# Optimization experiments

Hardware: AMD Instinct MI355X
Metric: run time of the kernel (lower is better)

Reference implementation:

```python
import jax, jax.numpy as jnp
import numpy as np

B, T_IN, T_OUT, F, H = 256, 336, 96, 32, 256


def _lstm_cell(x_t, h, c, Wih, Whh, b):
    # PyTorch gate order: input, forget, cell(g), output
    gates = x_t @ Wih.T + h @ Whh.T + b  # [B, 4H]
    i, f, g, o = jnp.split(gates, 4, axis=-1)
    c_new = jax.nn.sigmoid(f) * c + jax.nn.sigmoid(i) * jnp.tanh(g)
    h_new = jax.nn.sigmoid(o) * jnp.tanh(c_new)
    return h_new, c_new


def setup_inputs() -> dict:
    key = jax.random.key(0)
    ks = jax.random.split(key, 16)
    s = 0.05  # keep recurrence numerically tame
    g = lambda k, shape: (jax.random.normal(k, shape) * s).astype(jnp.float32)
    return {
        "x": jax.random.normal(ks[0], (B, T_IN, F), dtype=jnp.float32),
        "enc_Wih0": g(ks[1], (4 * H, F)),
        "enc_Whh0": g(ks[2], (4 * H, H)),
        "enc_b0": g(ks[3], (4 * H,)),
        "enc_Wih1": g(ks[4], (4 * H, H)),
        "enc_Whh1": g(ks[5], (4 * H, H)),
        "enc_b1": g(ks[6], (4 * H,)),
        "dec_Wih0": g(ks[7], (4 * H, F)),
        "dec_Whh0": g(ks[8], (4 * H, H)),
        "dec_b0": g(ks[9], (4 * H,)),
        "dec_Wih1": g(ks[10], (4 * H, H)),
        "dec_Whh1": g(ks[11], (4 * H, H)),
        "dec_b1": g(ks[12], (4 * H,)),
        "dec_Wout": g(ks[13], (F, H)),
        "dec_bout": g(ks[14], (F,)),
    }


def reference(x, enc_Wih0, enc_Whh0, enc_b0, enc_Wih1, enc_Whh1, enc_b1,
              dec_Wih0, dec_Whh0, dec_b0, dec_Wih1, dec_Whh1, dec_b1,
              dec_Wout, dec_bout):
    batch = x.shape[0]
    zeros = jnp.zeros((batch, H), dtype=x.dtype)

    # --- encoder: step-by-step 2-layer LSTM over input sequence ---
    def enc_step(carry, x_t):
        h0, c0, h1, c1 = carry
        h0, c0 = _lstm_cell(x_t, h0, c0, enc_Wih0, enc_Whh0, enc_b0)
        h1, c1 = _lstm_cell(h0, h1, c1, enc_Wih1, enc_Whh1, enc_b1)
        return (h0, c0, h1, c1), None

    xs = jnp.swapaxes(x, 0, 1)  # [T_IN, B, F]
    (h0, c0, h1, c1), _ = jax.lax.scan(enc_step, (zeros, zeros, zeros, zeros), xs)

    def dec_step(carry, _):
        h0, c0, h1, c1, y = carry
        h0, c0 = _lstm_cell(y, h0, c0, dec_Wih0, dec_Whh0, dec_b0)
        h1, c1 = _lstm_cell(h0, h1, c1, dec_Wih1, dec_Whh1, dec_b1)
        y = h1 @ dec_Wout.T + dec_bout  # project hidden -> feature dim
        return (h0, c0, h1, c1, y), y

    y0 = x[:, -1, :]  # [B, F]
    _, ys = jax.lax.scan(dec_step, (h0, c0, h1, c1, y0), None, length=T_OUT)
    return jnp.swapaxes(ys, 0, 1)  # [B, T_OUT, F]
```

## Files before the change

### kernel.cpp

```cpp
#include <hip/hip_runtime.h>
#include <hip/hip_bf16.h>

#define BB   256
#define TIN  336
#define TOUT 96
#define FF   32
#define HH   256

#define NGS 16
#define NBG 16
#define RPG 16
#define TPB 512

#define KB0 9
#define KB1 16
#define ASTRIDE 520
#define XSTRIDE 40

#define N_L0  (16*4*KB0*64*8)
#define N_L1  (16*4*KB1*64*8)
#define U_E0  0
#define U_E1  (U_E0 + N_L0)
#define U_D0  (U_E1 + N_L1)
#define U_D1  (U_D0 + N_L1)
#define U_END (U_D1 + N_L1)
#define HPAR  65536
#define U_H0  U_END
#define U_H1  (U_H0 + 2*HPAR)
#define U_HD  (U_H1 + 2*HPAR)
#define U_CTR (U_HD + 96*HPAR)
#define U_ZEND (U_CTR + 2048)

#define GATE(bias, g, r, cc) (bias[(g)*16 + (cc)] + pbuf[0][r][(g)*16 + (cc)] + pbuf[1][r][(g)*16 + (cc)])

typedef __bf16 bf16x8 __attribute__((ext_vector_type(8)));
typedef float  f32x4  __attribute__((ext_vector_type(4)));

__device__ __forceinline__ float sigf(float x) { return 1.f / (1.f + __expf(-x)); }
__device__ __forceinline__ float tanhfast(float x) { return 1.f - 2.f / (__expf(2.f * x) + 1.f); }
__device__ __forceinline__ unsigned short f2bf(float f) {
    union { float f; unsigned u; } v; v.f = f;
    unsigned r = v.u + 0x7FFF + ((v.u >> 16) & 1);
    return (unsigned short)(r >> 16);
}
__device__ __forceinline__ uint4 ldg_sc(const void* p) {
    uint4 v;
    asm volatile("global_load_dwordx4 %0, %1, off sc0 sc1\n\ts_waitcnt vmcnt(0)"
                 : "=v"(v) : "v"(p) : "memory");
    return v;
}
__device__ __forceinline__ void ldg_sc2(const void* p0, const void* p1, uint4& a, uint4& b) {
    asm volatile("global_load_dwordx4 %0, %2, off sc0 sc1\n\t"
                 "global_load_dwordx4 %1, %3, off sc0 sc1\n\t"
                 "s_waitcnt vmcnt(0)"
                 : "=v"(a), "=v"(b) : "v"(p0), "v"(p1) : "memory");
}

__global__ void prep_kernel(const float* __restrict__ eWih0, const float* __restrict__ eWhh0,
                            const float* __restrict__ eWih1, const float* __restrict__ eWhh1,
                            const float* __restrict__ dWih0, const float* __restrict__ dWhh0,
                            const float* __restrict__ dWih1, const float* __restrict__ dWhh1,
                            const float* __restrict__ Wout,  float* __restrict__ wsf)
{
    unsigned short* wsu = (unsigned short*)wsf;
    for (long u = (long)blockIdx.x * blockDim.x + threadIdx.x; u < (long)U_END;
         u += (long)gridDim.x * blockDim.x) {
        int region; long l;
        if (u < U_E1)      { region = 0; l = u - U_E0; }
        else if (u < U_D0) { region = 1; l = u - U_E1; }
        else if (u < U_D1) { region = 2; l = u - U_D0; }
        else               { region = 3; l = u - U_D1; }
        const int KB = (region == 0) ? KB0 : KB1;
        int j = (int)(l & 7), lane = (int)((l >> 3) & 63);
        long rem = l >> 9;
        int kb = (int)(rem % KB), q = (int)(rem / KB);
        int nt = q & 3, gi = q >> 2;
        int k  = kb * 32 + ((lane >> 4) << 3) + j;
        int gj = nt * 256 + gi * 16 + (lane & 15);
        float v;
        if (region == 0)      v = (k < 32)  ? eWih0[gj * 32 + k]  : eWhh0[gj * 256 + (k - 32)];
        else if (region == 1) v = (k < 256) ? eWih1[gj * 256 + k] : eWhh1[gj * 256 + (k - 256)];
        else if (region == 2) {
            if (k < 256) v = dWhh0[gj * 256 + k];
            else {
                float acc = 0.f; int kk = k - 256;
                #pragma unroll 8
                for (int f = 0; f < 32; ++f) acc += dWih0[gj * 32 + f] * Wout[f * 256 + kk];
                v = acc;
            }
        } else                v = (k < 256) ? dWih1[gj * 256 + k] : dWhh1[gj * 256 + (k - 256)];
        wsu[u] = f2bf(v);
    }
    for (long z = (long)blockIdx.x * blockDim.x + threadIdx.x; z < (long)(4 * HPAR);
         z += (long)gridDim.x * blockDim.x)
        wsu[U_H0 + z] = 0;
    for (long z = (long)blockIdx.x * blockDim.x + threadIdx.x; z < 2048;
         z += (long)gridDim.x * blockDim.x)
        wsu[U_CTR + z] = 0;
}

__global__ __launch_bounds__(TPB) void lstm_main(
    const float* __restrict__ x,
    const float* __restrict__ eb0, const float* __restrict__ eb1,
    const float* __restrict__ db0, const float* __restrict__ db1,
    const float* __restrict__ Wout, const float* __restrict__ bout,
    const float* __restrict__ dWih0,
    float* __restrict__ ws, float* __restrict__ out)
{
    const int gi = blockIdx.x >> 4;
    const int gb = blockIdx.x & 15;

    unsigned short* wsu = (unsigned short*)ws;
    const unsigned short* h0u = wsu + U_H0;
    const unsigned short* h1u = wsu + U_H1;
    const unsigned short* hdu = wsu + U_HD;
    unsigned* h0d = (unsigned*)(wsu + U_H0);
    unsigned* hdd = (unsigned*)(wsu + U_HD);
    unsigned* flg = (unsigned*)(wsu + U_CTR) + gb * 32;

    const int t  = threadIdx.x;
    const int wv = t >> 6;
    const int ln = t & 63;
    const int nt = wv & 3, w2 = wv >> 2;
    const int arow = ln & 15, ak = (ln >> 4) << 3;

    __shared__ __align__(16) unsigned short Atile[16 * ASTRIDE];
    __shared__ __align__(16) unsigned short Xtile[16 * XSTRIDE];
    __shared__ float pbuf[2][16][68];
    __shared__ float cst[2][16][16];
    __shared__ float sb[5][64];

    if (t < 64) {
        int gj = (t >> 4) * 256 + gi * 16 + (t & 15);
        sb[0][t] = eb0[gj]; sb[1][t] = eb1[gj]; sb[3][t] = db1[gj]; sb[4][t] = db0[gj];
        float be = db0[gj];
        #pragma unroll 8
        for (int f = 0; f < 32; ++f) be += dWih0[gj * 32 + f] * bout[f];
        sb[2][t] = be;
    }
    if (t < 256) { cst[0][t >> 4][t & 15] = 0.f; cst[1][t >> 4][t & 15] = 0.f; }

    bf16x8 B0[8], B1[8];
    const int kbs0 = w2 ? 4 : 0, kbn0 = w2 ? 5 : 4;
    const int kbs1 = w2 ? 8 : 0;
    auto loadB = [&](size_t ubase, int KB, int kbs, int kbn, bf16x8* Breg) {
        #pragma unroll
        for (int i = 0; i < 8; ++i)
            if (i < kbn)
                Breg[i] = *(const bf16x8*)(wsu + ubase +
                            ((size_t)(nt * KB + kbs + i) * 64 + ln) * 8);
    };

    int posts = 0;
    auto gsync = [&]() {
        ++posts;
        if (t == 0)
            __hip_atomic_store(flg + gi, (unsigned)posts, __ATOMIC_RELAXED,
                               __HIP_MEMORY_SCOPE_AGENT);
        if (wv == 0) {
            for (;;) {
                unsigned v = __hip_atomic_load(flg + (ln & 15), __ATOMIC_RELAXED,
                                               __HIP_MEMORY_SCOPE_AGENT);
                if (__all((int)(v >= (unsigned)posts))) break;
                __builtin_amdgcn_s_sleep(1);
            }
        }
        __syncthreads();
    };

    auto stageEnc = [&](const unsigned short* h0src, const unsigned short* h1src, int xs) {
        const int r = t >> 5, c8 = t & 31;
        uint4 a, b;
        ldg_sc2(h0src + (size_t)(gb * RPG + r) * 256 + c8 * 8,
                h1src + (size_t)(gb * RPG + r) * 256 + c8 * 8, a, b);
        float xv = 0.f;
        if (xs >= 0) xv = x[((size_t)(gb * RPG + r) * TIN + xs) * FF + c8];
        *(uint4*)(Atile + r * ASTRIDE + c8 * 8) = a;
        *(uint4*)(Atile + r * ASTRIDE + 256 + c8 * 8) = b;
        if (xs >= 0) Xtile[r * XSTRIDE + c8] = f2bf(xv);
    };
    auto stageOne = [&](const unsigned short* src, int colbase) {
        const int r = t >> 5, c8 = t & 31;
        uint4 a = ldg_sc(src + (size_t)(gb * RPG + r) * 256 + c8 * 8);
        *(uint4*)(Atile + r * ASTRIDE + colbase + c8 * 8) = a;
    };
    auto stageTwo = [&](const unsigned short* s0, int cb0, const unsigned short* s1, int cb1) {
        const int r = t >> 5, c8 = t & 31;
        uint4 a, b;
        ldg_sc2(s0 + (size_t)(gb * RPG + r) * 256 + c8 * 8,
                s1 + (size_t)(gb * RPG + r) * 256 + c8 * 8, a, b);
        *(uint4*)(Atile + r * ASTRIDE + cb0 + c8 * 8) = a;
        *(uint4*)(Atile + r * ASTRIDE + cb1 + c8 * 8) = b;
    };
    auto stageZero = [&](int colbase) {
        const int r = t >> 5, c8 = t & 31;
        uint4 z = {0u, 0u, 0u, 0u};
        *(uint4*)(Atile + r * ASTRIDE + colbase + c8 * 8) = z;
    };

    auto phase = [&](const bf16x8* Breg, int kbs, int kbn, bool withX, const float* bias,
                     int layer, unsigned* hdstDw, bool addY0) {
        f32x4 acc = {0.f, 0.f, 0.f, 0.f};
        #pragma unroll
        for (int i = 0; i < 8; ++i) {
            if (i < kbn) {
                const int kb = kbs + i;
                bf16x8 a;
                if (withX && kb == 0) a = *(const bf16x8*)(Xtile + arow * XSTRIDE + ak);
                else {
                    const int koff = (withX ? (kb - 1) : kb) * 32;
                    a = *(const bf16x8*)(Atile + arow * ASTRIDE + koff + ak);
                }
                acc = __builtin_amdgcn_mfma_f32_16x16x32_bf16(a, Breg[i], acc, 0, 0, 0);
            }
        }
        #pragma unroll
        for (int rg = 0; rg < 4; ++rg)
            pbuf[w2][(ln >> 4) * 4 + rg][nt * 16 + arow] = acc[rg];
        __syncthreads();
        if (t < 128) {
            const int r = t >> 3, c2 = t & 7;
            const int c0 = c2 * 2, c1 = c0 + 1;
            float xi0 = GATE(bias, 0, r, c0), xf0 = GATE(bias, 1, r, c0);
            float xg0 = GATE(bias, 2, r, c0), xo0 = GATE(bias, 3, r, c0);
            float xi1 = GATE(bias, 0, r, c1), xf1 = GATE(bias, 1, r, c1);
            float xg1 = GATE(bias, 2, r, c1), xo1 = GATE(bias, 3, r, c1);
            if (addY0) {
                const float* xp = x + ((size_t)(gb * RPG + r) * TIN + (TIN - 1)) * FF;
                float xr[32];
                #pragma unroll
                for (int f = 0; f < 32; ++f) xr[f] = xp[f];
                #pragma unroll
                for (int g = 0; g < 4; ++g) {
                    const float* w0 = dWih0 + (size_t)(g * 256 + gi * 16 + c0) * 32;
                    const float* w1 = dWih0 + (size_t)(g * 256 + gi * 16 + c1) * 32;
                    float a0 = 0.f, a1 = 0.f;
                    #pragma unroll
                    for (int f = 0; f < 32; ++f) {
                        a0 = fmaf(w0[f], xr[f], a0);
                        a1 = fmaf(w1[f], xr[f], a1);
                    }
                    if (g == 0) { xi0 += a0; xi1 += a1; }
                    else if (g == 1) { xf0 += a0; xf1 += a1; }
                    else if (g == 2) { xg0 += a0; xg1 += a1; }
                    else { xo0 += a0; xo1 += a1; }
                }
            }
            float ca = cst[layer][r][c0], cb = cst[layer][r][c1];
            float cn0 = sigf(xf0) * ca + sigf(xi0) * tanhfast(xg0);
            float cn1 = sigf(xf1) * cb + sigf(xi1) * tanhfast(xg1);
            cst[layer][r][c0] = cn0; cst[layer][r][c1] = cn1;
            float h0v = sigf(xo0) * tanhfast(cn0);
            float h1v = sigf(xo1) * tanhfast(cn1);
            unsigned pv = (unsigned)f2bf(h0v) | ((unsigned)f2bf(h1v) << 16);
            __hip_atomic_store(hdstDw + (size_t)(gb * RPG + r) * 128 + gi * 8 + c2, pv,
                               __ATOMIC_RELAXED, __HIP_MEMORY_SCOPE_AGENT);
        }
        __syncthreads();
    };

    loadB(U_E0 + (size_t)gi * 18432, KB0, kbs0, kbn0, B0);
    loadB(U_E1 + (size_t)gi * 32768, KB1, kbs1, 8,    B1);
    { const int r = t >> 5, c8 = t & 31;
      uint4 z = {0u, 0u, 0u, 0u};
      *(uint4*)(Atile + r * ASTRIDE + c8 * 8) = z;
      Xtile[r * XSTRIDE + c8] = f2bf(x[((size_t)(gb * RPG + r) * TIN) * FF + c8]); }
    __syncthreads();

    for (int s = 0; s < TIN; ++s) {
        const int rp = s & 1, wp = rp ^ 1;
        phase(B0, kbs0, kbn0, true, sb[0], 0, h0d + (size_t)wp * (HPAR / 2), false);
        gsync();
        stageEnc(h0u + (size_t)wp * HPAR, h1u + (size_t)rp * HPAR,
                 (s + 1 < TIN) ? s + 1 : -1);
        __syncthreads();
        phase(B1, kbs1, 8, false, sb[1], 1,
              (unsigned*)(wsu + U_H1) + (size_t)wp * (HPAR / 2), false);
    }

    loadB(U_D0 + (size_t)gi * 32768, KB1, kbs1, 8, B0);
    loadB(U_D1 + (size_t)gi * 32768, KB1, kbs1, 8, B1);

    for (int s = TIN; s < TIN + TOUT; ++s) {
        const int wp = (s & 1) ^ 1, td = s - TIN;
        gsync();
        if (td == 0) stageZero(256);
        else stageOne(hdu + (size_t)(td - 1) * HPAR, 256);
        __syncthreads();
        phase(B0, kbs1, 8, false, (td == 0) ? sb[4] : sb[2], 0,
              h0d + (size_t)wp * (HPAR / 2), td == 0);
        gsync();
        if (td == 0) stageTwo(h0u + (size_t)wp * HPAR, 0, h1u + 0 * HPAR, 256);
        else stageOne(h0u + (size_t)wp * HPAR, 0);
        __syncthreads();
        phase(B1, kbs1, 8, false, sb[3], 1, hdd + (size_t)td * (HPAR / 2), false);
    }

    gsync();

    {
        const int r = t >> 5, fq = (t >> 4) & 1, kc = t & 15;
        const int f = gi * 2 + fq;
        const float* wf = Wout + (size_t)f * 256 + kc * 16;
        float wreg[16];
        #pragma unroll
        for (int i = 0; i < 16; ++i) wreg[i] = wf[i];
        const float bo = bout[f];
        for (int td = 0; td < TOUT; ++td) {
            const unsigned short* hp = hdu + (size_t)td * HPAR +
                                       (size_t)(gb * RPG + r) * 256 + kc * 16;
            uint4 ua = *(const uint4*)hp;
            uint4 ub = *(const uint4*)(hp + 8);
            unsigned w[8] = {ua.x, ua.y, ua.z, ua.w, ub.x, ub.y, ub.z, ub.w};
            float a = 0.f;
            #pragma unroll
            for (int j = 0; j < 8; ++j) {
                a = fmaf(__uint_as_float(w[j] << 16),        wreg[2 * j],     a);
                a = fmaf(__uint_as_float(w[j] & 0xffff0000u), wreg[2 * j + 1], a);
            }
            #pragma unroll
            for (int off = 1; off < 16; off <<= 1) a += __shfl_xor(a, off, 64);
            if (kc == 0)
                out[((size_t)(gb * RPG + r) * TOUT + td) * FF + f] = a + bo;
        }
    }
}

extern "C" void kernel_launch(void* const* d_in, const int* in_sizes, int n_in,
                              void* d_out, int out_size, void* d_ws, size_t ws_size,
                              hipStream_t stream) {
    const float* x     = (const float*)d_in[0];
    const float* eWih0 = (const float*)d_in[1];
    const float* eWhh0 = (const float*)d_in[2];
    const float* eb0   = (const float*)d_in[3];
    const float* eWih1 = (const float*)d_in[4];
    const float* eWhh1 = (const float*)d_in[5];
    const float* eb1   = (const float*)d_in[6];
    const float* dWih0 = (const float*)d_in[7];
    const float* dWhh0 = (const float*)d_in[8];
    const float* db0   = (const float*)d_in[9];
    const float* dWih1 = (const float*)d_in[10];
    const float* dWhh1 = (const float*)d_in[11];
    const float* db1   = (const float*)d_in[12];
    const float* dWout = (const float*)d_in[13];
    const float* dbout = (const float*)d_in[14];
    float* ws = (float*)d_ws;
    float* out = (float*)d_out;

    prep_kernel<<<1024, 256, 0, stream>>>(eWih0, eWhh0, eWih1, eWhh1,
                                          dWih0, dWhh0, dWih1, dWhh1, dWout, ws);
    lstm_main<<<NGS * NBG, TPB, 0, stream>>>(x, eb0, eb1, db0, db1,
                                             dWout, dbout, dWih0, ws, out);
}
```

Before: 1.484 ms.

## Halve block size, keep full K per wave, fuse gate math in registers

Reduces each block from 512 to 256 threads, so each wave holds the full K-range of weights in registers (16 bf16x8 fragments per layer) instead of splitting K across two wave groups. The weight layout interleaves the four gates within each 16-column MFMA tile, letting each lane gather i/f/g/o with shuffles and update its cell state in registers. This removes the LDS partial-sum buffer and the __syncthreads around it. The grid sync becomes per-wave flags polled by all waves, the decoder's y0 input projection becomes an extra MFMA from prepacked weights, and staging loads are widened. In exchange it uses much more register pressure, scatters bf16 stores more finely, and puts more traffic on the flag polling.

After: 5.046 ms. +240.1%, slower.

```diff
diff --git a/kernel.cpp b/kernel.cpp
--- a/kernel.cpp
+++ b/kernel.cpp
@@ -10,28 +10,28 @@
 #define NGS 16
 #define NBG 16
 #define RPG 16
-#define TPB 512
+#define TPB 256
 
 #define KB0 9
 #define KB1 16
 #define ASTRIDE 520
 #define XSTRIDE 40
 
-#define N_L0  (16*4*KB0*64*8)
-#define N_L1  (16*4*KB1*64*8)
-#define U_E0  0
-#define U_E1  (U_E0 + N_L0)
-#define U_D0  (U_E1 + N_L1)
-#define U_D1  (U_D0 + N_L1)
-#define U_END (U_D1 + N_L1)
-#define HPAR  65536
-#define U_H0  U_END
-#define U_H1  (U_H0 + 2*HPAR)
-#define U_HD  (U_H1 + 2*HPAR)
-#define U_CTR (U_HD + 96*HPAR)
-#define U_ZEND (U_CTR + 2048)
-
-#define GATE(bias, g, r, cc) (bias[(g)*16 + (cc)] + pbuf[0][r][(g)*16 + (cc)] + pbuf[1][r][(g)*16 + (cc)])
+#define N_E0   294912
+#define N_K512 524288
+#define N_DX   32768
+#define U_E0   0
+#define U_E1   (U_E0 + N_E0)
+#define U_D0   (U_E1 + N_K512)
+#define U_D1   (U_D0 + N_K512)
+#define U_DX   (U_D1 + N_K512)
+#define U_END  (U_DX + N_DX)
+#define HPAR   65536
+#define U_H0   U_END
+#define U_H1   (U_H0 + 2*HPAR)
+#define U_HD   (U_H1 + 2*HPAR)
+#define U_CTR  (U_HD + 96*HPAR)
+#define U_ZEND (U_CTR + 4096)
 
 typedef __bf16 bf16x8 __attribute__((ext_vector_type(8)));
 typedef float  f32x4  __attribute__((ext_vector_type(4)));
@@ -43,17 +43,28 @@
     unsigned r = v.u + 0x7FFF + ((v.u >> 16) & 1);
     return (unsigned short)(r >> 16);
 }
-__device__ __forceinline__ uint4 ldg_sc(const void* p) {
-    uint4 v;
-    asm volatile("global_load_dwordx4 %0, %1, off sc0 sc1\n\ts_waitcnt vmcnt(0)"
-                 : "=v"(v) : "v"(p) : "memory");
-    return v;
+__device__ __forceinline__ float sel4(f32x4 a, int i) {
+    return i == 0 ? a[0] : (i == 1 ? a[1] : (i == 2 ? a[2] : a[3]));
+}
+__device__ __forceinline__ float pick4(float a0, float a1, float a2, float a3, int i) {
+    return i == 0 ? a0 : (i == 1 ? a1 : (i == 2 ? a2 : a3));
 }
 __device__ __forceinline__ void ldg_sc2(const void* p0, const void* p1, uint4& a, uint4& b) {
     asm volatile("global_load_dwordx4 %0, %2, off sc0 sc1\n\t"
                  "global_load_dwordx4 %1, %3, off sc0 sc1\n\t"
                  "s_waitcnt vmcnt(0)"
                  : "=v"(a), "=v"(b) : "v"(p0), "v"(p1) : "memory");
+}
+__device__ __forceinline__ void ldg_sc4(const void* p0, const void* p1,
+                                        const void* p2, const void* p3,
+                                        uint4& a, uint4& b, uint4& c, uint4& d) {
+    asm volatile("global_load_dwordx4 %0, %4, off sc0 sc1\n\t"
+                 "global_load_dwordx4 %1, %5, off sc0 sc1\n\t"
+                 "global_load_dwordx4 %2, %6, off sc0 sc1\n\t"
+                 "global_load_dwordx4 %3, %7, off sc0 sc1\n\t"
+                 "s_waitcnt vmcnt(0)"
+                 : "=v"(a), "=v"(b), "=v"(c), "=v"(d)
+                 : "v"(p0), "v"(p1), "v"(p2), "v"(p3) : "memory");
 }
 
 __global__ void prep_kernel(const float* __restrict__ eWih0, const float* __restrict__ eWhh0,
@@ -69,14 +80,17 @@
         if (u < U_E1)      { region = 0; l = u - U_E0; }
         else if (u < U_D0) { region = 1; l = u - U_E1; }
         else if (u < U_D1) { region = 2; l = u - U_D0; }
-        else               { region = 3; l = u - U_D1; }
-        const int KB = (region == 0) ? KB0 : KB1;
+        else if (u < U_DX) { region = 3; l = u - U_D1; }
+        else               { region = 4; l = u - U_DX; }
+        const int KB = (region == 0) ? KB0 : (region == 4 ? 1 : KB1);
         int j = (int)(l & 7), lane = (int)((l >> 3) & 63);
         long rem = l >> 9;
         int kb = (int)(rem % KB), q = (int)(rem / KB);
         int nt = q & 3, gi = q >> 2;
         int k  = kb * 32 + ((lane >> 4) << 3) + j;
-        int gj = nt * 256 + gi * 16 + (lane & 15);
+        int cl = lane & 15;
+        int gate = cl & 3, hh = nt * 4 + (cl >> 2);
+        int gj = gate * 256 + gi * 16 + hh;
         float v;
         if (region == 0)      v = (k < 32)  ? eWih0[gj * 32 + k]  : eWhh0[gj * 256 + (k - 32)];
         else if (region == 1) v = (k < 256) ? eWih1[gj * 256 + k] : eWhh1[gj * 256 + (k - 256)];
@@ -88,18 +102,20 @@
                 for (int f = 0; f < 32; ++f) acc += dWih0[gj * 32 + f] * Wout[f * 256 + kk];
                 v = acc;
             }
-        } else                v = (k < 256) ? dWih1[gj * 256 + k] : dWhh1[gj * 256 + (k - 256)];
+        }
+        else if (region == 3) v = (k < 256) ? dWih1[gj * 256 + k] : dWhh1[gj * 256 + (k - 256)];
+        else                  v = dWih0[gj * 32 + k];
         wsu[u] = f2bf(v);
     }
     for (long z = (long)blockIdx.x * blockDim.x + threadIdx.x; z < (long)(4 * HPAR);
          z += (long)gridDim.x * blockDim.x)
         wsu[U_H0 + z] = 0;
-    for (long z = (long)blockIdx.x * blockDim.x + threadIdx.x; z < 2048;
+    for (long z = (long)blockIdx.x * blockDim.x + threadIdx.x; z < 4096;
          z += (long)gridDim.x * blockDim.x)
         wsu[U_CTR + z] = 0;
 }
 
-__global__ __launch_bounds__(TPB) void lstm_main(
+__global__ __launch_bounds__(TPB, 1) void lstm_main(
     const float* __restrict__ x,
     const float* __restrict__ eb0, const float* __restrict__ eb1,
     const float* __restrict__ db0, const float* __restrict__ db1,
@@ -114,214 +130,203 @@
     const unsigned short* h0u = wsu + U_H0;
     const unsigned short* h1u = wsu + U_H1;
     const unsigned short* hdu = wsu + U_HD;
-    unsigned* h0d = (unsigned*)(wsu + U_H0);
-    unsigned* hdd = (unsigned*)(wsu + U_HD);
-    unsigned* flg = (unsigned*)(wsu + U_CTR) + gb * 32;
+    unsigned* flagbase = (unsigned*)(wsu + U_CTR) + gb * 64;
 
     const int t  = threadIdx.x;
     const int wv = t >> 6;
     const int ln = t & 63;
-    const int nt = wv & 3, w2 = wv >> 2;
+    const int nt = wv;
     const int arow = ln & 15, ak = (ln >> 4) << 3;
+    const int g = ln & 3;
+    const int hh = nt * 4 + ((ln >> 2) & 3);
+    const int myrow = gb * 16 + (ln >> 4) * 4 + g;
+    const int mycol = gi * 16 + hh;
 
     __shared__ __align__(16) unsigned short Atile[16 * ASTRIDE];
     __shared__ __align__(16) unsigned short Xtile[16 * XSTRIDE];
-    __shared__ float pbuf[2][16][68];
-    __shared__ float cst[2][16][16];
-    __shared__ float sb[5][64];
-
-    if (t < 64) {
-        int gj = (t >> 4) * 256 + gi * 16 + (t & 15);
-        sb[0][t] = eb0[gj]; sb[1][t] = eb1[gj]; sb[3][t] = db1[gj]; sb[4][t] = db0[gj];
+
+    float bE0[4], bE1[4], bD0p[4], bDe[4], bD1[4];
+    #pragma unroll
+    for (int gg = 0; gg < 4; ++gg) {
+        const int gj = gg * 256 + gi * 16 + hh;
+        bE0[gg] = eb0[gj]; bE1[gg] = eb1[gj]; bD0p[gg] = db0[gj]; bD1[gg] = db1[gj];
         float be = db0[gj];
         #pragma unroll 8
         for (int f = 0; f < 32; ++f) be += dWih0[gj * 32 + f] * bout[f];
-        sb[2][t] = be;
-    }
-    if (t < 256) { cst[0][t >> 4][t & 15] = 0.f; cst[1][t >> 4][t & 15] = 0.f; }
-
-    bf16x8 B0[8], B1[8];
-    const int kbs0 = w2 ? 4 : 0, kbn0 = w2 ? 5 : 4;
-    const int kbs1 = w2 ? 8 : 0;
-    auto loadB = [&](size_t ubase, int KB, int kbs, int kbn, bf16x8* Breg) {
-        #pragma unroll
-        for (int i = 0; i < 8; ++i)
-            if (i < kbn)
-                Breg[i] = *(const bf16x8*)(wsu + ubase +
-                            ((size_t)(nt * KB + kbs + i) * 64 + ln) * 8);
+        bDe[gg] = be;
+    }
+    float creg[2] = {0.f, 0.f};
+
+    bf16x8 Brg0[16], Brg1[16], Bx0;
+    auto loadB = [&](long ubase, int KB, bf16x8* B) {
+        for (int i = 0; i < KB; ++i)
+            B[i] = *(const bf16x8*)(wsu + ubase + ((long)(nt * KB + i) * 64 + ln) * 8);
     };
 
     int posts = 0;
     auto gsync = [&]() {
         ++posts;
-        if (t == 0)
-            __hip_atomic_store(flg + gi, (unsigned)posts, __ATOMIC_RELAXED,
-                               __HIP_MEMORY_SCOPE_AGENT);
-        if (wv == 0) {
-            for (;;) {
-                unsigned v = __hip_atomic_load(flg + (ln & 15), __ATOMIC_RELAXED,
-                                               __HIP_MEMORY_SCOPE_AGENT);
-                if (__all((int)(v >= (unsigned)posts))) break;
-                __builtin_amdgcn_s_sleep(1);
-            }
-        }
-        __syncthreads();
-    };
-
+        asm volatile("s_waitcnt vmcnt(0)" ::: "memory");
+        if (ln == 0)
+            __hip_atomic_store(flagbase + (gi * 4 + wv), (unsigned)posts,
+                               __ATOMIC_RELAXED, __HIP_MEMORY_SCOPE_AGENT);
+        for (;;) {
+            unsigned v = __hip_atomic_load(flagbase + ln, __ATOMIC_RELAXED,
+                                           __HIP_MEMORY_SCOPE_AGENT);
+            if (__all((int)(v >= (unsigned)posts))) break;
+            __builtin_amdgcn_s_sleep(1);
+        }
+    };
+
+    const int sr = t >> 4, sc16 = t & 15;
     auto stageEnc = [&](const unsigned short* h0src, const unsigned short* h1src, int xs) {
-        const int r = t >> 5, c8 = t & 31;
+        const unsigned short* p0 = h0src + (long)(gb * 16 + sr) * 256 + sc16 * 16;
+        const unsigned short* p1 = h1src + (long)(gb * 16 + sr) * 256 + sc16 * 16;
+        uint4 a, b, c, d;
+        ldg_sc4(p0, p0 + 8, p1, p1 + 8, a, b, c, d);
+        float2 xv = {0.f, 0.f};
+        if (xs >= 0) xv = *(const float2*)(x + ((long)(gb * 16 + sr) * TIN + xs) * FF + sc16 * 2);
+        *(uint4*)(Atile + sr * ASTRIDE + sc16 * 16) = a;
+        *(uint4*)(Atile + sr * ASTRIDE + sc16 * 16 + 8) = b;
+        *(uint4*)(Atile + sr * ASTRIDE + 256 + sc16 * 16) = c;
+        *(uint4*)(Atile + sr * ASTRIDE + 256 + sc16 * 16 + 8) = d;
+        if (xs >= 0) {
+            unsigned pv = (unsigned)f2bf(xv.x) | ((unsigned)f2bf(xv.y) << 16);
+            *(unsigned*)(Xtile + sr * XSTRIDE + sc16 * 2) = pv;
+        }
+    };
+    auto stageOne = [&](const unsigned short* src, int colbase) {
+        const unsigned short* p = src + (long)(gb * 16 + sr) * 256 + sc16 * 16;
         uint4 a, b;
-        ldg_sc2(h0src + (size_t)(gb * RPG + r) * 256 + c8 * 8,
-                h1src + (size_t)(gb * RPG + r) * 256 + c8 * 8, a, b);
-        float xv = 0.f;
-        if (xs >= 0) xv = x[((size_t)(gb * RPG + r) * TIN + xs) * FF + c8];
-        *(uint4*)(Atile + r * ASTRIDE + c8 * 8) = a;
-        *(uint4*)(Atile + r * ASTRIDE + 256 + c8 * 8) = b;
-        if (xs >= 0) Xtile[r * XSTRIDE + c8] = f2bf(xv);
-    };
-    auto stageOne = [&](const unsigned short* src, int colbase) {
-        const int r = t >> 5, c8 = t & 31;
-        uint4 a = ldg_sc(src + (size_t)(gb * RPG + r) * 256 + c8 * 8);
-        *(uint4*)(Atile + r * ASTRIDE + colbase + c8 * 8) = a;
+        ldg_sc2(p, p + 8, a, b);
+        *(uint4*)(Atile + sr * ASTRIDE + colbase + sc16 * 16) = a;
+        *(uint4*)(Atile + sr * ASTRIDE + colbase + sc16 * 16 + 8) = b;
     };
     auto stageTwo = [&](const unsigned short* s0, int cb0, const unsigned short* s1, int cb1) {
-        const int r = t >> 5, c8 = t & 31;
-        uint4 a, b;
-        ldg_sc2(s0 + (size_t)(gb * RPG + r) * 256 + c8 * 8,
-                s1 + (size_t)(gb * RPG + r) * 256 + c8 * 8, a, b);
-        *(uint4*)(Atile + r * ASTRIDE + cb0 + c8 * 8) = a;
-        *(uint4*)(Atile + r * ASTRIDE + cb1 + c8 * 8) = b;
+        const unsigned short* p0 = s0 + (long)(gb * 16 + sr) * 256 + sc16 * 16;
+        const unsigned short* p1 = s1 + (long)(gb * 16 + sr) * 256 + sc16 * 16;
+        uint4 a, b, c, d;
+        ldg_sc4(p0, p0 + 8, p1, p1 + 8, a, b, c, d);
+        *(uint4*)(Atile + sr * ASTRIDE + cb0 + sc16 * 16) = a;
+        *(uint4*)(Atile + sr * ASTRIDE + cb0 + sc16 * 16 + 8) = b;
+        *(uint4*)(Atile + sr * ASTRIDE + cb1 + sc16 * 16) = c;
+        *(uint4*)(Atile + sr * ASTRIDE + cb1 + sc16 * 16 + 8) = d;
     };
     auto stageZero = [&](int colbase) {
-        const int r = t >> 5, c8 = t & 31;
         uint4 z = {0u, 0u, 0u, 0u};
-        *(uint4*)(Atile + r * ASTRIDE + colbase + c8 * 8) = z;
-    };
-
-    auto phase = [&](const bf16x8* Breg, int kbs, int kbn, bool withX, const float* bias,
-                     int layer, unsigned* hdstDw, bool addY0) {
+        *(uint4*)(Atile + sr * ASTRIDE + colbase + sc16 * 16) = z;
+        *(uint4*)(Atile + sr * ASTRIDE + colbase + sc16 * 16 + 8) = z;
+    };
+    auto stageX = [&](int xs) {
+        float2 xv = *(const float2*)(x + ((long)(gb * 16 + sr) * TIN + xs) * FF + sc16 * 2);
+        unsigned pv = (unsigned)f2bf(xv.x) | ((unsigned)f2bf(xv.y) << 16);
+        *(unsigned*)(Xtile + sr * XSTRIDE + sc16 * 2) = pv;
+    };
+
+    auto phase = [&](const bf16x8* B, int KB, bool withX, const float* bias, int layer,
+                     unsigned short* hdst, bool addY0) {
         f32x4 acc = {0.f, 0.f, 0.f, 0.f};
         #pragma unroll
-        for (int i = 0; i < 8; ++i) {
-            if (i < kbn) {
-                const int kb = kbs + i;
+        for (int kb = 0; kb < 16; ++kb) {
+            if (kb < KB) {
                 bf16x8 a;
                 if (withX && kb == 0) a = *(const bf16x8*)(Xtile + arow * XSTRIDE + ak);
                 else {
                     const int koff = (withX ? (kb - 1) : kb) * 32;
                     a = *(const bf16x8*)(Atile + arow * ASTRIDE + koff + ak);
                 }
-                acc = __builtin_amdgcn_mfma_f32_16x16x32_bf16(a, Breg[i], acc, 0, 0, 0);
-            }
-        }
-        #pragma unroll
-        for (int rg = 0; rg < 4; ++rg)
-            pbuf[w2][(ln >> 4) * 4 + rg][nt * 16 + arow] = acc[rg];
-        __syncthreads();
-        if (t < 128) {
-            const int r = t >> 3, c2 = t & 7;
-            const int c0 = c2 * 2, c1 = c0 + 1;
-            float xi0 = GATE(bias, 0, r, c0), xf0 = GATE(bias, 1, r, c0);
-            float xg0 = GATE(bias, 2, r, c0), xo0 = GATE(bias, 3, r, c0);
-            float xi1 = GATE(bias, 0, r, c1), xf1 = GATE(bias, 1, r, c1);
-            float xg1 = GATE(bias, 2, r, c1), xo1 = GATE(bias, 3, r, c1);
-            if (addY0) {
-                const float* xp = x + ((size_t)(gb * RPG + r) * TIN + (TIN - 1)) * FF;
-                float xr[32];
-                #pragma unroll
-                for (int f = 0; f < 32; ++f) xr[f] = xp[f];
-                #pragma unroll
-                for (int g = 0; g < 4; ++g) {
-                    const float* w0 = dWih0 + (size_t)(g * 256 + gi * 16 + c0) * 32;
-                    const float* w1 = dWih0 + (size_t)(g * 256 + gi * 16 + c1) * 32;
-                    float a0 = 0.f, a1 = 0.f;
-                    #pragma unroll
-                    for (int f = 0; f < 32; ++f) {
-                        a0 = fmaf(w0[f], xr[f], a0);
-                        a1 = fmaf(w1[f], xr[f], a1);
-                    }
-                    if (g == 0) { xi0 += a0; xi1 += a1; }
-                    else if (g == 1) { xf0 += a0; xf1 += a1; }
-                    else if (g == 2) { xg0 += a0; xg1 += a1; }
-                    else { xo0 += a0; xo1 += a1; }
-                }
-            }
-            float ca = cst[layer][r][c0], cb = cst[layer][r][c1];
-            float cn0 = sigf(xf0) * ca + sigf(xi0) * tanhfast(xg0);
-            float cn1 = sigf(xf1) * cb + sigf(xi1) * tanhfast(xg1);
-            cst[layer][r][c0] = cn0; cst[layer][r][c1] = cn1;
-            float h0v = sigf(xo0) * tanhfast(cn0);
-            float h1v = sigf(xo1) * tanhfast(cn1);
-            unsigned pv = (unsigned)f2bf(h0v) | ((unsigned)f2bf(h1v) << 16);
-            __hip_atomic_store(hdstDw + (size_t)(gb * RPG + r) * 128 + gi * 8 + c2, pv,
-                               __ATOMIC_RELAXED, __HIP_MEMORY_SCOPE_AGENT);
-        }
-        __syncthreads();
-    };
-
-    loadB(U_E0 + (size_t)gi * 18432, KB0, kbs0, kbn0, B0);
-    loadB(U_E1 + (size_t)gi * 32768, KB1, kbs1, 8,    B1);
-    { const int r = t >> 5, c8 = t & 31;
-      uint4 z = {0u, 0u, 0u, 0u};
-      *(uint4*)(Atile + r * ASTRIDE + c8 * 8) = z;
-      Xtile[r * XSTRIDE + c8] = f2bf(x[((size_t)(gb * RPG + r) * TIN) * FF + c8]); }
+                acc = __builtin_amdgcn_mfma_f32_16x16x32_bf16(a, B[kb], acc, 0, 0, 0);
+            }
+        }
+        if (addY0) {
+            bf16x8 a = *(const bf16x8*)(Xtile + arow * XSTRIDE + ak);
+            acc = __builtin_amdgcn_mfma_f32_16x16x32_bf16(a, Bx0, acc, 0, 0, 0);
+        }
+        float own = sel4(acc, g);
+        float t1 = __shfl_xor(sel4(acc, g ^ 1), 1);
+        float t2 = __shfl_xor(sel4(acc, g ^ 2), 2);
+        float t3 = __shfl_xor(sel4(acc, g ^ 3), 3);
+        float xi = pick4(own, t1, t2, t3, g)     + bias[0];
+        float xf = pick4(own, t1, t2, t3, g ^ 1) + bias[1];
+        float xg = pick4(own, t1, t2, t3, g ^ 2) + bias[2];
+        float xo = pick4(own, t1, t2, t3, g ^ 3) + bias[3];
+        float c  = creg[layer];
+        float cn = sigf(xf) * c + sigf(xi) * tanhfast(xg);
+        creg[layer] = cn;
+        float hv = sigf(xo) * tanhfast(cn);
+        __hip_atomic_store(hdst + (long)myrow * 256 + mycol, f2bf(hv),
+                           __ATOMIC_RELAXED, __HIP_MEMORY_SCOPE_AGENT);
+    };
+
+    loadB(U_E0 + (long)gi * 18432, KB0, Brg0);
+    loadB(U_E1 + (long)gi * 32768, KB1, Brg1);
+    stageZero(0);
+    stageX(0);
     __syncthreads();
 
     for (int s = 0; s < TIN; ++s) {
         const int rp = s & 1, wp = rp ^ 1;
-        phase(B0, kbs0, kbn0, true, sb[0], 0, h0d + (size_t)wp * (HPAR / 2), false);
+        phase(Brg0, KB0, true, bE0, 0, wsu + U_H0 + (long)wp * HPAR, false);
         gsync();
-        stageEnc(h0u + (size_t)wp * HPAR, h1u + (size_t)rp * HPAR,
-                 (s + 1 < TIN) ? s + 1 : -1);
+        stageEnc(h0u + (long)wp * HPAR, h1u + (long)rp * HPAR, (s + 1 < TIN) ? s + 1 : -1);
         __syncthreads();
-        phase(B1, kbs1, 8, false, sb[1], 1,
-              (unsigned*)(wsu + U_H1) + (size_t)wp * (HPAR / 2), false);
-    }
-
-    loadB(U_D0 + (size_t)gi * 32768, KB1, kbs1, 8, B0);
-    loadB(U_D1 + (size_t)gi * 32768, KB1, kbs1, 8, B1);
+        phase(Brg1, KB1, false, bE1, 1, wsu + U_H1 + (long)wp * HPAR, false);
+    }
+
+    loadB(U_D0 + (long)gi * 32768, KB1, Brg0);
+    loadB(U_D1 + (long)gi * 32768, KB1, Brg1);
+    Bx0 = *(const bf16x8*)(wsu + U_DX + (long)gi * 2048 + ((long)nt * 64 + ln) * 8);
+    stageX(TIN - 1);
 
     for (int s = TIN; s < TIN + TOUT; ++s) {
         const int wp = (s & 1) ^ 1, td = s - TIN;
         gsync();
         if (td == 0) stageZero(256);
-        else stageOne(hdu + (size_t)(td - 1) * HPAR, 256);
+        else stageOne(hdu + (long)(td - 1) * HPAR, 256);
         __syncthreads();
-        phase(B0, kbs1, 8, false, (td == 0) ? sb[4] : sb[2], 0,
-              h0d + (size_t)wp * (HPAR / 2), td == 0);
+        phase(Brg0, KB1, false, (td == 0) ? bD0p : bDe, 0,
+              wsu + U_H0 + (long)wp * HPAR, td == 0);
         gsync();
-        if (td == 0) stageTwo(h0u + (size_t)wp * HPAR, 0, h1u + 0 * HPAR, 256);
-        else stageOne(h0u + (size_t)wp * HPAR, 0);
+        if (td == 0) stageTwo(h0u + (long)wp * HPAR, 0, h1u + 0 * HPAR, 256);
+        else stageOne(h0u + (long)wp * HPAR, 0);
         __syncthreads();
-        phase(B1, kbs1, 8, false, sb[3], 1, hdd + (size_t)td * (HPAR / 2), false);
+        phase(Brg1, KB1, false, bD1, 1, wsu + U_HD + (long)td * HPAR, false);
     }
 
     gsync();
 
     {
-        const int r = t >> 5, fq = (t >> 4) & 1, kc = t & 15;
-        const int f = gi * 2 + fq;
-        const float* wf = Wout + (size_t)f * 256 + kc * 16;
-        float wreg[16];
+        const int r = t >> 4, kc = t & 15;
+        const int f0 = gi * 2, f1 = f0 + 1;
+        float w0[16], w1[16];
         #pragma unroll
-        for (int i = 0; i < 16; ++i) wreg[i] = wf[i];
-        const float bo = bout[f];
+        for (int i = 0; i < 16; ++i) {
+            w0[i] = Wout[(long)f0 * 256 + kc * 16 + i];
+            w1[i] = Wout[(long)f1 * 256 + kc * 16 + i];
+        }
+        const float bo0 = bout[f0], bo1 = bout[f1];
         for (int td = 0; td < TOUT; ++td) {
-            const unsigned short* hp = hdu + (size_t)td * HPAR +
-                                       (size_t)(gb * RPG + r) * 256 + kc * 16;
+            const unsigned short* hp = hdu + (long)td * HPAR + (long)(gb * 16 + r) * 256 + kc * 16;
             uint4 ua = *(const uint4*)hp;
             uint4 ub = *(const uint4*)(hp + 8);
-            unsigned w[8] = {ua.x, ua.y, ua.z, ua.w, ub.x, ub.y, ub.z, ub.w};
-            float a = 0.f;
+            unsigned wds[8] = {ua.x, ua.y, ua.z, ua.w, ub.x, ub.y, ub.z, ub.w};
+            float a0 = 0.f, a1 = 0.f;
             #pragma unroll
             for (int j = 0; j < 8; ++j) {
-                a = fmaf(__uint_as_float(w[j] << 16),        wreg[2 * j],     a);
-                a = fmaf(__uint_as_float(w[j] & 0xffff0000u), wreg[2 * j + 1], a);
+                float lo = __uint_as_float(wds[j] << 16);
+                float hi = __uint_as_float(wds[j] & 0xffff0000u);
+                a0 = fmaf(lo, w0[2 * j], a0); a0 = fmaf(hi, w0[2 * j + 1], a0);
+                a1 = fmaf(lo, w1[2 * j], a1); a1 = fmaf(hi, w1[2 * j + 1], a1);
             }
             #pragma unroll
-            for (int off = 1; off < 16; off <<= 1) a += __shfl_xor(a, off, 64);
-            if (kc == 0)
-                out[((size_t)(gb * RPG + r) * TOUT + td) * FF + f] = a + bo;
+            for (int off = 1; off < 16; off <<= 1) {
+                a0 += __shfl_xor(a0, off);
+                a1 += __shfl_xor(a1, off);
+            }
+            if (kc == 0) {
+                float2 yv = {a0 + bo0, a1 + bo1};
+                *(float2*)(out + ((long)(gb * 16 + r) * TOUT + td) * FF + f0) = yv;
+            }
         }
     }
 }
```
